# Performance work log

Hardware: AMD Instinct MI355X
Metric: run time of the kernel (lower is better)

Reference implementation:

```python
import jax, jax.numpy as jnp
import numpy as np

B, C, D, L, CTX = 8, 320, 24, 77, 768
NUM_GROUPS = 32
EPS = 1e-5


def setup_inputs() -> dict:
    key = jax.random.key(0)
    ks = jax.random.split(key, 8)
    s = 0.02
    return {
        "x": jax.random.normal(ks[0], (B, C, D, D, D), jnp.float32),
        "context": jax.random.normal(ks[1], (B, L, CTX), jnp.float32),
        "Wq": jax.random.normal(ks[2], (C, C), jnp.float32) * s,
        "bq": jnp.zeros((C,), jnp.float32),
        "Wk": jax.random.normal(ks[3], (C, CTX), jnp.float32) * s,
        "bk": jnp.zeros((C,), jnp.float32),
        "Wv": jax.random.normal(ks[4], (C, CTX), jnp.float32) * s,
        "bv": jnp.zeros((C,), jnp.float32),
        "Wo": jax.random.normal(ks[5], (C, C), jnp.float32) * s,
        "bo": jnp.zeros((C,), jnp.float32),
        "gamma": jnp.ones((C,), jnp.float32),
        "beta": jnp.zeros((C,), jnp.float32),
    }


def reference(x, context, Wq, bq, Wk, bk, Wv, bv, Wo, bo, gamma, beta):
    b, c = x.shape[:2]
    spatial = x.shape[2:]
    xf = x.reshape(b, c, -1)                                # [B, C, N]
    # 1x1 Conv3d == per-position channel matmul
    q = jnp.einsum('oc,bcn->bon', Wq, xf) + bq[None, :, None]
    ctx_t = context.transpose(0, 2, 1)                      # [B, CTX, L]
    k = jnp.einsum('oc,bcl->bol', Wk, ctx_t) + bk[None, :, None]
    v = jnp.einsum('oc,bcl->bol', Wv, ctx_t) + bv[None, :, None]
    # scores [B, N, L], scaled by C^-0.5 (int(C) in the original)
    qk = jnp.einsum('bcn,bcl->bnl', q, k) * (float(c) ** -0.5)
    w = jax.nn.softmax(qk, axis=-1)
    h = jnp.einsum('bcl,bnl->bcn', v, w)                    # [B, C, N]
    h = jnp.einsum('oc,bcn->bon', Wo, h) + bo[None, :, None]
    xr = h + xf                                             # residual
    # GroupNorm over (C/G, spatial) per group
    g = NUM_GROUPS
    xg = xr.reshape(b, g, -1)
    mu = jnp.mean(xg, axis=-1, keepdims=True)
    var = jnp.var(xg, axis=-1, keepdims=True)
    xn = ((xg - mu) * jax.lax.rsqrt(var + EPS)).reshape(b, c, -1)
    xn = xn * gamma[None, :, None] + beta[None, :, None]
    out = xn * jax.nn.sigmoid(xn)                           # Swish
    return out.reshape(b, c, *spatial)
```

## Files before the change

### kernel.cpp

```cpp
#include <hip/hip_runtime.h>
#include <hip/hip_bf16.h>

#define B_ 8
#define C_ 320
#define N_ 13824
#define NT 128
#define L_ 77
#define LP 80
#define LV 96
#define CTXD 768
#define CPG 10
#define EPS_ 1e-5f
#define SCALE_ 0.05590169943749474f
#define WTP 120

typedef __attribute__((__ext_vector_type__(4))) float f32x4;
typedef __attribute__((__ext_vector_type__(8))) short s16x8;

#define WS_ACCUM 0
#define WS_T     2048
#define WS_KST   4608
#define WS_VST   414208
#define WS_K2T   823808
#define WS_V2    1233408
#define WS_WQT   1724928
#define WS_WO    1929728

__device__ __forceinline__ unsigned short f2bf(float f) {
  union { float f; unsigned u; } v; v.f = f;
  unsigned r = v.u + 0x7FFFu + ((v.u >> 16) & 1u);
  return (unsigned short)(r >> 16);
}
__device__ __forceinline__ float bf2f(unsigned short s) {
  union { unsigned u; float f; } v; v.u = ((unsigned)s) << 16;
  return v.f;
}
__device__ __forceinline__ s16x8 cvt8(const float* p) {
  f32x4 a = *reinterpret_cast<const f32x4*>(p);
  f32x4 b = *reinterpret_cast<const f32x4*>(p + 4);
  s16x8 r;
  r[0] = (short)f2bf(a[0]); r[1] = (short)f2bf(a[1]);
  r[2] = (short)f2bf(a[2]); r[3] = (short)f2bf(a[3]);
  r[4] = (short)f2bf(b[0]); r[5] = (short)f2bf(b[1]);
  r[6] = (short)f2bf(b[2]); r[7] = (short)f2bf(b[3]);
  return r;
}
__device__ __forceinline__ f32x4 MFMA(s16x8 a, s16x8 b, f32x4 c) {
  return __builtin_amdgcn_mfma_f32_16x16x32_bf16(a, b, c, 0, 0, 0);
}

__global__ __launch_bounds__(256) void prep_kernel(const float* __restrict__ Wq,
                                                   const float* __restrict__ Wo,
                                                   const float* __restrict__ ctx,
                                                   const float* __restrict__ Wk,
                                                   const float* __restrict__ bk,
                                                   const float* __restrict__ Wv,
                                                   const float* __restrict__ bv,
                                                   unsigned short* __restrict__ wqT,
                                                   unsigned short* __restrict__ wo_bf,
                                                   unsigned short* __restrict__ kst,
                                                   unsigned short* __restrict__ vst,
                                                   float* __restrict__ zws) {
  int bid = blockIdx.x;
  if (bid < 400) {
    int t = bid * 256 + threadIdx.x;
    if (t >= C_ * C_) return;
    int o = t / C_, c = t - o * C_;
    wqT[c * C_ + o] = f2bf(Wq[t]);
    wo_bf[t] = f2bf(Wo[t]);
    return;
  }
  int kb = bid - 400;
  { int t = kb * 256 + threadIdx.x; if (t < 1152) zws[t] = 0.f; }
  int lt = kb % 5;
  int kb5 = kb / 5;
  int b = kb5 / 5;
  int oc = kb5 % 5;
  int w = threadIdx.x >> 6, lane = threadIdx.x & 63;
  int r = lane & 15, h = lane >> 4;
  int o_row = oc * 64 + w * 16 + r;
  int l = lt * 16 + r;
  bool lok = (l < L_);
  f32x4 ak = {}, av = {};
  for (int ks = 0; ks < 24; ++ks) {
    int c0 = ks * 32 + h * 8;
    s16x8 aWk = cvt8(Wk + o_row * CTXD + c0);
    s16x8 aWv = cvt8(Wv + o_row * CTXD + c0);
    s16x8 bfr = {0,0,0,0,0,0,0,0};
    if (lok) bfr = cvt8(ctx + (b * L_ + l) * CTXD + c0);
    ak = MFMA(aWk, bfr, ak);
    av = MFMA(aWv, bfr, av);
  }
#pragma unroll
  for (int j = 0; j < 4; ++j) {
    int o = oc * 64 + w * 16 + h * 4 + j;
    float bkv = bk[o], bvv = bv[o];
    unsigned short kw = lok ? f2bf(SCALE_ * (ak[j] + bkv)) : (unsigned short)0;
    unsigned short vw = lok ? f2bf(av[j] + bvv) : (unsigned short)0;
    kst[(b * LP + l) * C_ + o] = kw;
    vst[(b * LP + l) * C_ + o] = vw;
  }
}

__global__ __launch_bounds__(256) void kv2_kernel(const unsigned short* __restrict__ wqT,
                                                  const unsigned short* __restrict__ wo_bf,
                                                  const unsigned short* __restrict__ kst,
                                                  const unsigned short* __restrict__ vst,
                                                  const float* __restrict__ bq,
                                                  float* __restrict__ tbuf,
                                                  unsigned short* __restrict__ k2T,
                                                  unsigned short* __restrict__ v2) {
  int b = blockIdx.x / 5;
  int cc = blockIdx.x % 5;
  int w = threadIdx.x >> 6, lane = threadIdx.x & 63;
  int r = lane & 15, h = lane >> 4;
  int c_row = cc * 64 + w * 16 + r;
  f32x4 a2[5] = {}, av[5] = {};
#pragma unroll
  for (int ks = 0; ks < 10; ++ks) {
    int o0 = ks * 32 + h * 8;
    s16x8 aq = *reinterpret_cast<const s16x8*>(wqT + c_row * C_ + o0);
    s16x8 ao = *reinterpret_cast<const s16x8*>(wo_bf + c_row * C_ + o0);
#pragma unroll
    for (int nt = 0; nt < 5; ++nt) {
      int l = nt * 16 + r;
      s16x8 bk_ = *reinterpret_cast<const s16x8*>(kst + (b * LP + l) * C_ + o0);
      s16x8 bv_ = *reinterpret_cast<const s16x8*>(vst + (b * LP + l) * C_ + o0);
      a2[nt] = MFMA(aq, bk_, a2[nt]);
      av[nt] = MFMA(ao, bv_, av[nt]);
    }
  }
#pragma unroll
  for (int j = 0; j < 4; ++j) {
    int c = cc * 64 + w * 16 + h * 4 + j;
#pragma unroll
    for (int nt = 0; nt < 5; ++nt) {
      int l = nt * 16 + r;
      k2T[(b * LP + l) * C_ + c] = f2bf(a2[nt][j]);
      v2[(b * C_ + c) * LV + l] = f2bf(av[nt][j]);
    }
  }
  {
    int c = cc * 64 + w * 16 + (lane >> 2);
    int l = 80 + (lane & 3) * 4;
    unsigned long long* p = (unsigned long long*)(v2 + ((long)(b * C_ + c)) * LV + l);
    *p = 0ull;
  }
  if (cc == 0 && threadIdx.x < LP) {
    int l = threadIdx.x;
    float acc = 0.f;
    for (int o8 = 0; o8 < C_; o8 += 8) {
      s16x8 kv = *reinterpret_cast<const s16x8*>(kst + (b * LP + l) * C_ + o8);
#pragma unroll
      for (int j = 0; j < 8; ++j) acc += bq[o8 + j] * bf2f((unsigned short)kv[j]);
    }
    tbuf[b * LP + l] = acc;
  }
}

__global__ __launch_bounds__(512, 3) void main_kernel(const float* __restrict__ x,
                                                      const unsigned short* __restrict__ k2T,
                                                      const unsigned short* __restrict__ v2,
                                                      const float* __restrict__ tbuf,
                                                      const float* __restrict__ bo,
                                                      float* __restrict__ accum,
                                                      float* __restrict__ hout) {
  __shared__ __align__(16) unsigned short wT[NT][WTP];
  __shared__ float ch[2][C_][2];
  int bid = blockIdx.x;
  int swz = (bid & 7) * 108 + (bid >> 3);
  int b = swz / 108;
  int n0 = (swz % 108) * NT;
  int tid = threadIdx.x;
  int w = tid >> 6, lane = tid & 63, r = lane & 15, h = lane >> 4;
  const float* xg = x + (long)b * C_ * N_ + n0;
  const unsigned short* k2b = k2T + (long)b * LP * C_;
  const float* xrow = xg + w * 16 + r;

  f32x4 sacc[5] = {};
  float xvA[8], xvB[8];
#pragma unroll
  for (int j = 0; j < 8; ++j) xvA[j] = xrow[(long)(h * 8 + j) * N_];
#pragma unroll
  for (int j = 0; j < 8; ++j) xvB[j] = xrow[(long)(32 + h * 8 + j) * N_];

#define SCHUNK(KS, XV)                                                          \
  {                                                                             \
    s16x8 a;                                                                    \
    _Pragma("unroll") for (int j = 0; j < 8; ++j) a[j] = (short)f2bf(XV[j]);    \
    if (KS < 8) {                                                               \
      _Pragma("unroll") for (int j = 0; j < 8; ++j)                             \
          XV[j] = xrow[(long)((KS + 2) * 32 + h * 8 + j) * N_];                 \
    }                                                                           \
    _Pragma("unroll") for (int nt = 0; nt < 5; ++nt) {                          \
      s16x8 kf = *reinterpret_cast<const s16x8*>(                               \
          k2b + (nt * 16 + r) * C_ + KS * 32 + h * 8);                          \
      sacc[nt] = MFMA(a, kf, sacc[nt]);                                         \
    }                                                                           \
  }
  SCHUNK(0, xvA) SCHUNK(1, xvB) SCHUNK(2, xvA) SCHUNK(3, xvB) SCHUNK(4, xvA)
  SCHUNK(5, xvB) SCHUNK(6, xvA) SCHUNK(7, xvB) SCHUNK(8, xvA) SCHUNK(9, xvB)
#undef SCHUNK

#pragma unroll
  for (int nt = 0; nt < 5; ++nt) {
    float tl = tbuf[b * LP + nt * 16 + r];
#pragma unroll
    for (int j = 0; j < 4; ++j) sacc[nt][j] += tl;
  }
  bool maskpad = (r >= 13);
#pragma unroll
  for (int j = 0; j < 4; ++j) {
    float m = -1e30f;
#pragma unroll
    for (int nt = 0; nt < 5; ++nt) {
      float v = (nt == 4 && maskpad) ? -1e30f : sacc[nt][j];
      m = fmaxf(m, v);
    }
    for (int d = 1; d < 16; d <<= 1) m = fmaxf(m, __shfl_xor(m, d));
    float e[5]; float sum = 0.f;
#pragma unroll
    for (int nt = 0; nt < 5; ++nt) {
      float v = (nt == 4 && maskpad) ? 0.f : __expf(sacc[nt][j] - m);
      e[nt] = v; sum += v;
    }
    for (int d = 1; d < 16; d <<= 1) sum += __shfl_xor(sum, d);
    float inv = 1.f / sum;
    int n = w * 16 + h * 4 + j;
#pragma unroll
    for (int nt = 0; nt < 5; ++nt) wT[n][nt * 16 + r] = f2bf(e[nt] * inv);
  }
  {
    int row = tid >> 2, c0 = 80 + (tid & 3) * 4;
    *reinterpret_cast<unsigned*>(&wT[row][c0]) = 0u;
    *reinterpret_cast<unsigned*>(&wT[row][c0 + 2]) = 0u;
  }
  __syncthreads();

  int nh = w >> 2;
  int cc4 = w & 3;
  f32x4 acc[5][4] = {};
#pragma unroll
  for (int ks = 0; ks < 3; ++ks) {
    int l0 = ks * 32 + h * 8;
    s16x8 bfr[4];
#pragma unroll
    for (int nt = 0; nt < 4; ++nt)
      bfr[nt] = *reinterpret_cast<const s16x8*>(&wT[nh * 64 + nt * 16 + r][l0]);
#pragma unroll
    for (int mt = 0; mt < 5; ++mt) {
      int c = cc4 * 80 + mt * 16 + r;
      s16x8 a = *reinterpret_cast<const s16x8*>(v2 + ((long)(b * C_ + c)) * LV + l0);
#pragma unroll
      for (int nt = 0; nt < 4; ++nt) acc[mt][nt] = MFMA(a, bfr[nt], acc[mt][nt]);
    }
  }
#pragma unroll
  for (int mt = 0; mt < 5; ++mt) {
    int cb = cc4 * 80 + mt * 16 + h * 4;
    float bov[4];
#pragma unroll
    for (int j = 0; j < 4; ++j) bov[j] = bo[cb + j];
    float sv[4] = {0.f, 0.f, 0.f, 0.f}, sq[4] = {0.f, 0.f, 0.f, 0.f};
#pragma unroll
    for (int nt = 0; nt < 4; ++nt) {
      int n = nh * 64 + nt * 16 + r;
      const float* xp = xg + (long)cb * N_ + n;
#pragma unroll
      for (int j = 0; j < 4; ++j) {
        float val = acc[mt][nt][j] + bov[j] + xp[(long)j * N_];
        long e = ((long)b * C_ + cb + j) * N_ + n0 + n;
        *reinterpret_cast<unsigned short*>(
            (char*)hout + ((e >> 11) << 13) + ((e & 2047) << 1)) = f2bf(val);
        sv[j] += val; sq[j] += val * val;
      }
    }
#pragma unroll
    for (int j = 0; j < 4; ++j) {
      for (int d = 1; d < 16; d <<= 1) {
        sv[j] += __shfl_xor(sv[j], d);
        sq[j] += __shfl_xor(sq[j], d);
      }
      if (r == 0) { ch[nh][cb + j][0] = sv[j]; ch[nh][cb + j][1] = sq[j]; }
    }
  }
  __syncthreads();
  if (tid < 32) {
    float s0 = 0.f, s1 = 0.f;
#pragma unroll
    for (int i = 0; i < CPG; ++i) {
      int c = tid * CPG + i;
      s0 += ch[0][c][0] + ch[1][c][0];
      s1 += ch[0][c][1] + ch[1][c][1];
    }
    atomicAdd(&accum[b * 64 + tid * 2], s0);
    atomicAdd(&accum[b * 64 + tid * 2 + 1], s1);
  }
}

__global__ __launch_bounds__(256) void norm_kernel(float* __restrict__ hout,
                                                   const float* __restrict__ accum,
                                                   const float* __restrict__ gamma,
                                                   const float* __restrict__ beta) {
  long idx0 = (long)blockIdx.x * 2048;
  int t = threadIdx.x;
  s16x8 hv = *reinterpret_cast<const s16x8*>((const char*)hout + idx0 * 4 + t * 16);
  __syncthreads();
  long idx = idx0 + (long)t * 8;
  int b = (int)(idx / ((long)C_ * N_));
  long rem = idx - (long)b * C_ * N_;
  int c = (int)(rem / N_);
  int g = c / CPG;
  float s0 = accum[b * 64 + g * 2], s1 = accum[b * 64 + g * 2 + 1];
  const float invc = 1.f / 138240.f;
  float mu = s0 * invc;
  float var = s1 * invc - mu * mu;
  float rstd = rsqrtf(var + EPS_);
  float ga = gamma[c], be = beta[c];
  f32x4 v0, v1;
#pragma unroll
  for (int q = 0; q < 4; ++q) {
    float y = (bf2f((unsigned short)hv[q]) - mu) * rstd * ga + be;
    v0[q] = y / (1.f + __expf(-y));
    float z = (bf2f((unsigned short)hv[q + 4]) - mu) * rstd * ga + be;
    v1[q] = z / (1.f + __expf(-z));
  }
  *reinterpret_cast<f32x4*>(hout + idx) = v0;
  *reinterpret_cast<f32x4*>(hout + idx + 4) = v1;
}

extern "C" void kernel_launch(void* const* d_in, const int* in_sizes, int n_in,
                              void* d_out, int out_size, void* d_ws, size_t ws_size,
                              hipStream_t stream) {
  const float* x     = (const float*)d_in[0];
  const float* ctx   = (const float*)d_in[1];
  const float* Wq    = (const float*)d_in[2];
  const float* bq    = (const float*)d_in[3];
  const float* Wk    = (const float*)d_in[4];
  const float* bk    = (const float*)d_in[5];
  const float* Wv    = (const float*)d_in[6];
  const float* bv    = (const float*)d_in[7];
  const float* Wo    = (const float*)d_in[8];
  const float* bo    = (const float*)d_in[9];
  const float* gamma = (const float*)d_in[10];
  const float* beta  = (const float*)d_in[11];
  float* out = (float*)d_out;
  char* ws = (char*)d_ws;

  float* accum = (float*)(ws + WS_ACCUM);
  float* tbuf  = (float*)(ws + WS_T);
  unsigned short* kst  = (unsigned short*)(ws + WS_KST);
  unsigned short* vst  = (unsigned short*)(ws + WS_VST);
  unsigned short* k2T  = (unsigned short*)(ws + WS_K2T);
  unsigned short* v2   = (unsigned short*)(ws + WS_V2);
  unsigned short* wqT  = (unsigned short*)(ws + WS_WQT);
  unsigned short* wo_b = (unsigned short*)(ws + WS_WO);

  prep_kernel<<<dim3(600), dim3(256), 0, stream>>>(Wq, Wo, ctx, Wk, bk, Wv, bv,
                                                   wqT, wo_b, kst, vst, (float*)ws);
  kv2_kernel<<<dim3(40), dim3(256), 0, stream>>>(wqT, wo_b, kst, vst, bq, tbuf, k2T, v2);
  main_kernel<<<dim3(864), dim3(512), 0, stream>>>(x, k2T, v2, tbuf, bo, accum, out);
  norm_kernel<<<dim3(17280), dim3(256), 0, stream>>>(out, accum, gamma, beta);
}
```

Baseline: 194.4 us.

## Software-pipeline x, K and V loads and prefetch residual tiles in fused attention kernel

Deepens the software pipeline in the score GEMM by triple-buffering x rows and double-buffering K fragments in registers, so global loads are issued one or two chunks ahead of the MFMAs that use them. In the PV GEMM, the next V fragment is loaded before the current MFMAs run. The residual x values are prefetched into registers, with the first tile loaded before the barrier and later tiles double-buffered across the epilogue loop. The aim is to hide global memory latency behind compute, at the cost of many more live registers, which may reduce occupancy or cause spills.

```diff
diff --git a/kernel.cpp b/kernel.cpp
--- a/kernel.cpp
+++ b/kernel.cpp
@@ -178,28 +178,38 @@
   const float* xrow = xg + w * 16 + r;
 
   f32x4 sacc[5] = {};
-  float xvA[8], xvB[8];
-#pragma unroll
-  for (int j = 0; j < 8; ++j) xvA[j] = xrow[(long)(h * 8 + j) * N_];
-#pragma unroll
-  for (int j = 0; j < 8; ++j) xvB[j] = xrow[(long)(32 + h * 8 + j) * N_];
-
-#define SCHUNK(KS, XV)                                                          \
-  {                                                                             \
-    s16x8 a;                                                                    \
-    _Pragma("unroll") for (int j = 0; j < 8; ++j) a[j] = (short)f2bf(XV[j]);    \
-    if (KS < 8) {                                                               \
-      _Pragma("unroll") for (int j = 0; j < 8; ++j)                             \
-          XV[j] = xrow[(long)((KS + 2) * 32 + h * 8 + j) * N_];                 \
-    }                                                                           \
-    _Pragma("unroll") for (int nt = 0; nt < 5; ++nt) {                          \
-      s16x8 kf = *reinterpret_cast<const s16x8*>(                               \
-          k2b + (nt * 16 + r) * C_ + KS * 32 + h * 8);                          \
-      sacc[nt] = MFMA(a, kf, sacc[nt]);                                         \
-    }                                                                           \
-  }
-  SCHUNK(0, xvA) SCHUNK(1, xvB) SCHUNK(2, xvA) SCHUNK(3, xvB) SCHUNK(4, xvA)
-  SCHUNK(5, xvB) SCHUNK(6, xvA) SCHUNK(7, xvB) SCHUNK(8, xvA) SCHUNK(9, xvB)
+  float xv0[8], xv1[8], xv2[8];
+#pragma unroll
+  for (int j = 0; j < 8; ++j) xv0[j] = xrow[(long)(h * 8 + j) * N_];
+#pragma unroll
+  for (int j = 0; j < 8; ++j) xv1[j] = xrow[(long)(32 + h * 8 + j) * N_];
+#pragma unroll
+  for (int j = 0; j < 8; ++j) xv2[j] = xrow[(long)(64 + h * 8 + j) * N_];
+  s16x8 kfA[5], kfB[5];
+#pragma unroll
+  for (int nt = 0; nt < 5; ++nt)
+    kfA[nt] = *reinterpret_cast<const s16x8*>(k2b + (nt * 16 + r) * C_ + h * 8);
+
+#define SCHUNK(KS, XV, KC, KN)                                                   \
+  {                                                                              \
+    s16x8 a;                                                                     \
+    _Pragma("unroll") for (int j = 0; j < 8; ++j) a[j] = (short)f2bf(XV[j]);     \
+    if (KS < 7) {                                                                \
+      _Pragma("unroll") for (int j = 0; j < 8; ++j)                              \
+          XV[j] = xrow[(long)((KS + 3) * 32 + h * 8 + j) * N_];                  \
+    }                                                                            \
+    if (KS < 9) {                                                                \
+      _Pragma("unroll") for (int nt = 0; nt < 5; ++nt)                           \
+          KN[nt] = *reinterpret_cast<const s16x8*>(                              \
+              k2b + (nt * 16 + r) * C_ + (KS + 1) * 32 + h * 8);                 \
+    }                                                                            \
+    _Pragma("unroll") for (int nt = 0; nt < 5; ++nt)                             \
+      sacc[nt] = MFMA(a, KC[nt], sacc[nt]);                                      \
+  }
+  SCHUNK(0, xv0, kfA, kfB) SCHUNK(1, xv1, kfB, kfA) SCHUNK(2, xv2, kfA, kfB)
+  SCHUNK(3, xv0, kfB, kfA) SCHUNK(4, xv1, kfA, kfB) SCHUNK(5, xv2, kfB, kfA)
+  SCHUNK(6, xv0, kfA, kfB) SCHUNK(7, xv1, kfB, kfA) SCHUNK(8, xv2, kfA, kfB)
+  SCHUNK(9, xv0, kfB, kfA)
 #undef SCHUNK
 
 #pragma unroll
@@ -235,11 +245,21 @@
     *reinterpret_cast<unsigned*>(&wT[row][c0]) = 0u;
     *reinterpret_cast<unsigned*>(&wT[row][c0 + 2]) = 0u;
   }
-  __syncthreads();
 
   int nh = w >> 2;
   int cc4 = w & 3;
+  float rs0[16], rs1[16];
+#pragma unroll
+  for (int nt = 0; nt < 4; ++nt)
+#pragma unroll
+    for (int j = 0; j < 4; ++j)
+      rs0[nt * 4 + j] =
+          xg[(long)(cc4 * 80 + h * 4 + j) * N_ + nh * 64 + nt * 16 + r];
+  __syncthreads();
+
+  const unsigned short* v2b = v2 + (long)b * C_ * LV;
   f32x4 acc[5][4] = {};
+  s16x8 va = *reinterpret_cast<const s16x8*>(v2b + (long)(cc4 * 80 + r) * LV + h * 8);
 #pragma unroll
   for (int ks = 0; ks < 3; ++ks) {
     int l0 = ks * 32 + h * 8;
@@ -249,14 +269,30 @@
       bfr[nt] = *reinterpret_cast<const s16x8*>(&wT[nh * 64 + nt * 16 + r][l0]);
 #pragma unroll
     for (int mt = 0; mt < 5; ++mt) {
-      int c = cc4 * 80 + mt * 16 + r;
-      s16x8 a = *reinterpret_cast<const s16x8*>(v2 + ((long)(b * C_ + c)) * LV + l0);
-#pragma unroll
-      for (int nt = 0; nt < 4; ++nt) acc[mt][nt] = MFMA(a, bfr[nt], acc[mt][nt]);
+      s16x8 vn;
+      if (!(ks == 2 && mt == 4)) {
+        int ks2 = (mt == 4) ? ks + 1 : ks;
+        int mt2 = (mt == 4) ? 0 : mt + 1;
+        vn = *reinterpret_cast<const s16x8*>(
+            v2b + (long)(cc4 * 80 + mt2 * 16 + r) * LV + ks2 * 32 + h * 8);
+      }
+#pragma unroll
+      for (int nt = 0; nt < 4; ++nt) acc[mt][nt] = MFMA(va, bfr[nt], acc[mt][nt]);
+      if (!(ks == 2 && mt == 4)) va = vn;
     }
   }
 #pragma unroll
   for (int mt = 0; mt < 5; ++mt) {
+    float* rc = (mt & 1) ? rs1 : rs0;
+    float* rn = (mt & 1) ? rs0 : rs1;
+    if (mt < 4) {
+#pragma unroll
+      for (int nt = 0; nt < 4; ++nt)
+#pragma unroll
+        for (int j = 0; j < 4; ++j)
+          rn[nt * 4 + j] = xg[(long)(cc4 * 80 + (mt + 1) * 16 + h * 4 + j) * N_ +
+                              nh * 64 + nt * 16 + r];
+    }
     int cb = cc4 * 80 + mt * 16 + h * 4;
     float bov[4];
 #pragma unroll
@@ -265,10 +301,9 @@
 #pragma unroll
     for (int nt = 0; nt < 4; ++nt) {
       int n = nh * 64 + nt * 16 + r;
-      const float* xp = xg + (long)cb * N_ + n;
 #pragma unroll
       for (int j = 0; j < 4; ++j) {
-        float val = acc[mt][nt][j] + bov[j] + xp[(long)j * N_];
+        float val = acc[mt][nt][j] + bov[j] + rc[nt * 4 + j];
         long e = ((long)b * C_ + cb + j) * N_ + n0 + n;
         *reinterpret_cast<unsigned short*>(
             (char*)hout + ((e >> 11) << 13) + ((e & 2047) << 1)) = f2bf(val);
```

Result: slower. 206.9 us (+6.4%).

## Shrink main kernel to single-wave blocks of sixteen positions each

Applied to the files above, without the earlier changes.

The attention main kernel is restructured from 512-thread blocks covering 128 positions into 64-thread single-wave blocks covering 16 positions, launched as 6912 blocks. This removes the block-level __syncthreads and the two-stage shared-memory reduction, and each wave computes all 320 output channels for its positions. In exchange, the k2T and v2 operands are reloaded from global memory by eight times as many blocks. Group-statistic atomics also rise eightfold, and the explicit software prefetch of x is dropped.

```diff
diff --git a/kernel.cpp b/kernel.cpp
--- a/kernel.cpp
+++ b/kernel.cpp
@@ -4,7 +4,7 @@
 #define B_ 8
 #define C_ 320
 #define N_ 13824
-#define NT 128
+#define NB 16
 #define L_ 77
 #define LP 80
 #define LV 96
@@ -158,49 +158,36 @@
   }
 }
 
-__global__ __launch_bounds__(512, 3) void main_kernel(const float* __restrict__ x,
-                                                      const unsigned short* __restrict__ k2T,
-                                                      const unsigned short* __restrict__ v2,
-                                                      const float* __restrict__ tbuf,
-                                                      const float* __restrict__ bo,
-                                                      float* __restrict__ accum,
-                                                      float* __restrict__ hout) {
-  __shared__ __align__(16) unsigned short wT[NT][WTP];
-  __shared__ float ch[2][C_][2];
+__global__ __launch_bounds__(64, 3) void main_kernel(const float* __restrict__ x,
+                                                     const unsigned short* __restrict__ k2T,
+                                                     const unsigned short* __restrict__ v2,
+                                                     const float* __restrict__ tbuf,
+                                                     const float* __restrict__ bo,
+                                                     float* __restrict__ accum,
+                                                     float* __restrict__ hout) {
+  __shared__ __align__(16) unsigned short wT[NB][WTP];
+  __shared__ float ch[C_][2];
   int bid = blockIdx.x;
-  int swz = (bid & 7) * 108 + (bid >> 3);
-  int b = swz / 108;
-  int n0 = (swz % 108) * NT;
-  int tid = threadIdx.x;
-  int w = tid >> 6, lane = tid & 63, r = lane & 15, h = lane >> 4;
+  int b = bid & 7;
+  int n0 = (bid >> 3) * NB;
+  int lane = threadIdx.x & 63, r = lane & 15, h = lane >> 4;
   const float* xg = x + (long)b * C_ * N_ + n0;
   const unsigned short* k2b = k2T + (long)b * LP * C_;
-  const float* xrow = xg + w * 16 + r;
+  const unsigned short* v2b = v2 + (long)b * C_ * LV;
+  const float* xrow = xg + r;
 
   f32x4 sacc[5] = {};
-  float xvA[8], xvB[8];
-#pragma unroll
-  for (int j = 0; j < 8; ++j) xvA[j] = xrow[(long)(h * 8 + j) * N_];
-#pragma unroll
-  for (int j = 0; j < 8; ++j) xvB[j] = xrow[(long)(32 + h * 8 + j) * N_];
-
-#define SCHUNK(KS, XV)                                                          \
-  {                                                                             \
-    s16x8 a;                                                                    \
-    _Pragma("unroll") for (int j = 0; j < 8; ++j) a[j] = (short)f2bf(XV[j]);    \
-    if (KS < 8) {                                                               \
-      _Pragma("unroll") for (int j = 0; j < 8; ++j)                             \
-          XV[j] = xrow[(long)((KS + 2) * 32 + h * 8 + j) * N_];                 \
-    }                                                                           \
-    _Pragma("unroll") for (int nt = 0; nt < 5; ++nt) {                          \
-      s16x8 kf = *reinterpret_cast<const s16x8*>(                               \
-          k2b + (nt * 16 + r) * C_ + KS * 32 + h * 8);                          \
-      sacc[nt] = MFMA(a, kf, sacc[nt]);                                         \
-    }                                                                           \
-  }
-  SCHUNK(0, xvA) SCHUNK(1, xvB) SCHUNK(2, xvA) SCHUNK(3, xvB) SCHUNK(4, xvA)
-  SCHUNK(5, xvB) SCHUNK(6, xvA) SCHUNK(7, xvB) SCHUNK(8, xvA) SCHUNK(9, xvB)
-#undef SCHUNK
+#pragma unroll
+  for (int ks = 0; ks < 10; ++ks) {
+    s16x8 a;
+#pragma unroll
+    for (int j = 0; j < 8; ++j) a[j] = (short)f2bf(xrow[(long)(ks * 32 + h * 8 + j) * N_]);
+#pragma unroll
+    for (int nt = 0; nt < 5; ++nt) {
+      s16x8 kf = *reinterpret_cast<const s16x8*>(k2b + (nt * 16 + r) * C_ + ks * 32 + h * 8);
+      sacc[nt] = MFMA(a, kf, sacc[nt]);
+    }
+  }
 
 #pragma unroll
   for (int nt = 0; nt < 5; ++nt) {
@@ -226,75 +213,56 @@
     }
     for (int d = 1; d < 16; d <<= 1) sum += __shfl_xor(sum, d);
     float inv = 1.f / sum;
-    int n = w * 16 + h * 4 + j;
+    int n = h * 4 + j;
 #pragma unroll
     for (int nt = 0; nt < 5; ++nt) wT[n][nt * 16 + r] = f2bf(e[nt] * inv);
   }
   {
-    int row = tid >> 2, c0 = 80 + (tid & 3) * 4;
-    *reinterpret_cast<unsigned*>(&wT[row][c0]) = 0u;
-    *reinterpret_cast<unsigned*>(&wT[row][c0 + 2]) = 0u;
-  }
-  __syncthreads();
-
-  int nh = w >> 2;
-  int cc4 = w & 3;
-  f32x4 acc[5][4] = {};
-#pragma unroll
-  for (int ks = 0; ks < 3; ++ks) {
-    int l0 = ks * 32 + h * 8;
-    s16x8 bfr[4];
-#pragma unroll
-    for (int nt = 0; nt < 4; ++nt)
-      bfr[nt] = *reinterpret_cast<const s16x8*>(&wT[nh * 64 + nt * 16 + r][l0]);
-#pragma unroll
-    for (int mt = 0; mt < 5; ++mt) {
-      int c = cc4 * 80 + mt * 16 + r;
-      s16x8 a = *reinterpret_cast<const s16x8*>(v2 + ((long)(b * C_ + c)) * LV + l0);
-#pragma unroll
-      for (int nt = 0; nt < 4; ++nt) acc[mt][nt] = MFMA(a, bfr[nt], acc[mt][nt]);
-    }
-  }
-#pragma unroll
-  for (int mt = 0; mt < 5; ++mt) {
-    int cb = cc4 * 80 + mt * 16 + h * 4;
-    float bov[4];
-#pragma unroll
-    for (int j = 0; j < 4; ++j) bov[j] = bo[cb + j];
-    float sv[4] = {0.f, 0.f, 0.f, 0.f}, sq[4] = {0.f, 0.f, 0.f, 0.f};
-#pragma unroll
-    for (int nt = 0; nt < 4; ++nt) {
-      int n = nh * 64 + nt * 16 + r;
-      const float* xp = xg + (long)cb * N_ + n;
+    int row = lane >> 2, c0 = 80 + (lane & 3) * 4;
+    *reinterpret_cast<unsigned long long*>(&wT[row][c0]) = 0ull;
+  }
+
+#pragma unroll
+  for (int half = 0; half < 2; ++half) {
+    f32x4 acc[10] = {};
+#pragma unroll
+    for (int ks = 0; ks < 3; ++ks) {
+      s16x8 bfr = *reinterpret_cast<const s16x8*>(&wT[r][ks * 32 + h * 8]);
+#pragma unroll
+      for (int ct = 0; ct < 10; ++ct) {
+        int c = half * 160 + ct * 16 + r;
+        s16x8 va = *reinterpret_cast<const s16x8*>(v2b + (long)c * LV + ks * 32 + h * 8);
+        acc[ct] = MFMA(va, bfr, acc[ct]);
+      }
+    }
+#pragma unroll
+    for (int ct = 0; ct < 10; ++ct) {
+      int cb = half * 160 + ct * 16 + h * 4;
+      float sv[4], sq[4];
 #pragma unroll
       for (int j = 0; j < 4; ++j) {
-        float val = acc[mt][nt][j] + bov[j] + xp[(long)j * N_];
-        long e = ((long)b * C_ + cb + j) * N_ + n0 + n;
+        float val = acc[ct][j] + bo[cb + j] + xg[(long)(cb + j) * N_ + r];
+        long e = ((long)b * C_ + cb + j) * N_ + n0 + r;
         *reinterpret_cast<unsigned short*>(
             (char*)hout + ((e >> 11) << 13) + ((e & 2047) << 1)) = f2bf(val);
-        sv[j] += val; sq[j] += val * val;
+        sv[j] = val; sq[j] = val * val;
       }
-    }
-#pragma unroll
-    for (int j = 0; j < 4; ++j) {
-      for (int d = 1; d < 16; d <<= 1) {
-        sv[j] += __shfl_xor(sv[j], d);
-        sq[j] += __shfl_xor(sq[j], d);
+#pragma unroll
+      for (int j = 0; j < 4; ++j) {
+        for (int d = 1; d < 16; d <<= 1) {
+          sv[j] += __shfl_xor(sv[j], d);
+          sq[j] += __shfl_xor(sq[j], d);
+        }
+        if (r == 0) { ch[cb + j][0] = sv[j]; ch[cb + j][1] = sq[j]; }
       }
-      if (r == 0) { ch[nh][cb + j][0] = sv[j]; ch[nh][cb + j][1] = sq[j]; }
-    }
-  }
-  __syncthreads();
-  if (tid < 32) {
+    }
+  }
+  if (lane < 32) {
     float s0 = 0.f, s1 = 0.f;
 #pragma unroll
-    for (int i = 0; i < CPG; ++i) {
-      int c = tid * CPG + i;
-      s0 += ch[0][c][0] + ch[1][c][0];
-      s1 += ch[0][c][1] + ch[1][c][1];
-    }
-    atomicAdd(&accum[b * 64 + tid * 2], s0);
-    atomicAdd(&accum[b * 64 + tid * 2 + 1], s1);
+    for (int i = 0; i < CPG; ++i) { s0 += ch[lane * CPG + i][0]; s1 += ch[lane * CPG + i][1]; }
+    atomicAdd(&accum[b * 64 + lane * 2], s0);
+    atomicAdd(&accum[b * 64 + lane * 2 + 1], s1);
   }
 }
 
@@ -359,6 +327,6 @@
   prep_kernel<<<dim3(600), dim3(256), 0, stream>>>(Wq, Wo, ctx, Wk, bk, Wv, bv,
                                                    wqT, wo_b, kst, vst, (float*)ws);
   kv2_kernel<<<dim3(40), dim3(256), 0, stream>>>(wqT, wo_b, kst, vst, bq, tbuf, k2T, v2);
-  main_kernel<<<dim3(864), dim3(512), 0, stream>>>(x, k2T, v2, tbuf, bo, accum, out);
+  main_kernel<<<dim3(6912), dim3(64), 0, stream>>>(x, k2T, v2, tbuf, bo, accum, out);
   norm_kernel<<<dim3(17280), dim3(256), 0, stream>>>(out, accum, gamma, beta);
 }
```

Result: slower. 214.5 us (+10.3%).

## Pre-transpose x to bf16 position-major layout and fragment-order K for main kernel

Applied to the files above, without the earlier changes.

Adds a separate kernel that converts x to bf16 and transposes it to [B, N, C], so the main kernel reads contiguous 16-byte MFMA A-fragments instead of strided fp32 column loads. K2 is written in MFMA fragment order and double-buffered in registers, and V fragment loads are software-prefetched one step ahead. The residual now uses the bf16 copy of x, which lowers its precision. The extra pass reads all of x once and writes a bf16 copy, adding traffic and a launch, and the occupancy hint changes to waves_per_eu(2,3).

```diff
diff --git a/kernel.cpp b/kernel.cpp
--- a/kernel.cpp
+++ b/kernel.cpp
@@ -16,15 +16,17 @@
 
 typedef __attribute__((__ext_vector_type__(4))) float f32x4;
 typedef __attribute__((__ext_vector_type__(8))) short s16x8;
+typedef __attribute__((__ext_vector_type__(4))) unsigned short u16x4;
 
 #define WS_ACCUM 0
 #define WS_T     2048
 #define WS_KST   4608
 #define WS_VST   414208
-#define WS_K2T   823808
+#define WS_K2F   823808
 #define WS_V2    1233408
 #define WS_WQT   1724928
 #define WS_WO    1929728
+#define WS_XT    2134528
 
 __device__ __forceinline__ unsigned short f2bf(float f) {
   union { float f; unsigned u; } v; v.f = f;
@@ -47,6 +49,31 @@
 }
 __device__ __forceinline__ f32x4 MFMA(s16x8 a, s16x8 b, f32x4 c) {
   return __builtin_amdgcn_mfma_f32_16x16x32_bf16(a, b, c, 0, 0, 0);
+}
+
+__global__ __launch_bounds__(256) void xpose_kernel(const float* __restrict__ x,
+                                                    unsigned short* __restrict__ xT) {
+  __shared__ __align__(16) unsigned short tile[64][336];
+  int bid = blockIdx.x;
+  int b = bid & 7;
+  int t0 = (bid >> 3) * 64;
+  int tid = threadIdx.x;
+  int nq = (tid & 15) * 4;
+  int cc = tid >> 4;
+  const float* xb = x + (long)b * C_ * N_ + t0;
+#pragma unroll
+  for (int it = 0; it < 20; ++it) {
+    int c = it * 16 + cc;
+    f32x4 v = *reinterpret_cast<const f32x4*>(xb + (long)c * N_ + nq);
+#pragma unroll
+    for (int q = 0; q < 4; ++q) tile[nq + q][c] = f2bf(v[q]);
+  }
+  __syncthreads();
+  int row = tid >> 2, part = tid & 3;
+  const s16x8* src = reinterpret_cast<const s16x8*>(&tile[row][part * 80]);
+  s16x8* dst = reinterpret_cast<s16x8*>(xT + ((long)b * N_ + t0 + row) * C_ + part * 80);
+#pragma unroll
+  for (int k = 0; k < 10; ++k) dst[k] = src[k];
 }
 
 __global__ __launch_bounds__(256) void prep_kernel(const float* __restrict__ Wq,
@@ -108,7 +135,7 @@
                                                   const unsigned short* __restrict__ vst,
                                                   const float* __restrict__ bq,
                                                   float* __restrict__ tbuf,
-                                                  unsigned short* __restrict__ k2T,
+                                                  unsigned short* __restrict__ k2F,
                                                   unsigned short* __restrict__ v2) {
   int b = blockIdx.x / 5;
   int cc = blockIdx.x % 5;
@@ -133,10 +160,11 @@
 #pragma unroll
   for (int j = 0; j < 4; ++j) {
     int c = cc * 64 + w * 16 + h * 4 + j;
+    int ks2 = c >> 5, h2 = (c >> 3) & 3, j2 = c & 7;
 #pragma unroll
     for (int nt = 0; nt < 5; ++nt) {
       int l = nt * 16 + r;
-      k2T[(b * LP + l) * C_ + c] = f2bf(a2[nt][j]);
+      k2F[(((b * 5 + nt) * 10 + ks2) << 9) + ((h2 * 16 + r) << 3) + j2] = f2bf(a2[nt][j]);
       v2[(b * C_ + c) * LV + l] = f2bf(av[nt][j]);
     }
   }
@@ -158,13 +186,15 @@
   }
 }
 
-__global__ __launch_bounds__(512, 3) void main_kernel(const float* __restrict__ x,
-                                                      const unsigned short* __restrict__ k2T,
-                                                      const unsigned short* __restrict__ v2,
-                                                      const float* __restrict__ tbuf,
-                                                      const float* __restrict__ bo,
-                                                      float* __restrict__ accum,
-                                                      float* __restrict__ hout) {
+__global__ __launch_bounds__(512)
+__attribute__((amdgpu_waves_per_eu(2, 3)))
+void main_kernel(const unsigned short* __restrict__ xT,
+                 const unsigned short* __restrict__ k2F,
+                 const unsigned short* __restrict__ v2,
+                 const float* __restrict__ tbuf,
+                 const float* __restrict__ bo,
+                 float* __restrict__ accum,
+                 float* __restrict__ hout) {
   __shared__ __align__(16) unsigned short wT[NT][WTP];
   __shared__ float ch[2][C_][2];
   int bid = blockIdx.x;
@@ -173,33 +203,31 @@
   int n0 = (swz % 108) * NT;
   int tid = threadIdx.x;
   int w = tid >> 6, lane = tid & 63, r = lane & 15, h = lane >> 4;
-  const float* xg = x + (long)b * C_ * N_ + n0;
-  const unsigned short* k2b = k2T + (long)b * LP * C_;
-  const float* xrow = xg + w * 16 + r;
+  const unsigned short* xTb = xT + ((long)b * N_ + n0) * C_;
+  const unsigned short* xTn = xTb + (long)(w * 16 + r) * C_;
+  const unsigned short* k2f = k2F + ((long)b * 50 << 9);
 
   f32x4 sacc[5] = {};
-  float xvA[8], xvB[8];
-#pragma unroll
-  for (int j = 0; j < 8; ++j) xvA[j] = xrow[(long)(h * 8 + j) * N_];
-#pragma unroll
-  for (int j = 0; j < 8; ++j) xvB[j] = xrow[(long)(32 + h * 8 + j) * N_];
-
-#define SCHUNK(KS, XV)                                                          \
+  s16x8 kfA[5], kfB[5];
+#pragma unroll
+  for (int nt = 0; nt < 5; ++nt)
+    kfA[nt] = *reinterpret_cast<const s16x8*>(k2f + ((nt * 10) << 9) + (lane << 3));
+
+#define SCHUNK(KS, KC, KN)                                                      \
   {                                                                             \
-    s16x8 a;                                                                    \
-    _Pragma("unroll") for (int j = 0; j < 8; ++j) a[j] = (short)f2bf(XV[j]);    \
-    if (KS < 8) {                                                               \
-      _Pragma("unroll") for (int j = 0; j < 8; ++j)                             \
-          XV[j] = xrow[(long)((KS + 2) * 32 + h * 8 + j) * N_];                 \
+    s16x8 a = *reinterpret_cast<const s16x8*>(xTn + KS * 32 + h * 8);           \
+    if (KS < 9) {                                                               \
+      _Pragma("unroll") for (int nt = 0; nt < 5; ++nt)                          \
+          KN[nt] = *reinterpret_cast<const s16x8*>(                             \
+              k2f + ((nt * 10 + KS + 1) << 9) + (lane << 3));                   \
     }                                                                           \
-    _Pragma("unroll") for (int nt = 0; nt < 5; ++nt) {                          \
-      s16x8 kf = *reinterpret_cast<const s16x8*>(                               \
-          k2b + (nt * 16 + r) * C_ + KS * 32 + h * 8);                          \
-      sacc[nt] = MFMA(a, kf, sacc[nt]);                                         \
-    }                                                                           \
-  }
-  SCHUNK(0, xvA) SCHUNK(1, xvB) SCHUNK(2, xvA) SCHUNK(3, xvB) SCHUNK(4, xvA)
-  SCHUNK(5, xvB) SCHUNK(6, xvA) SCHUNK(7, xvB) SCHUNK(8, xvA) SCHUNK(9, xvB)
+    _Pragma("unroll") for (int nt = 0; nt < 5; ++nt)                            \
+      sacc[nt] = MFMA(a, KC[nt], sacc[nt]);                                     \
+  }
+  SCHUNK(0, kfA, kfB) SCHUNK(1, kfB, kfA) SCHUNK(2, kfA, kfB)
+  SCHUNK(3, kfB, kfA) SCHUNK(4, kfA, kfB) SCHUNK(5, kfB, kfA)
+  SCHUNK(6, kfA, kfB) SCHUNK(7, kfB, kfA) SCHUNK(8, kfA, kfB)
+  SCHUNK(9, kfB, kfA)
 #undef SCHUNK
 
 #pragma unroll
@@ -239,7 +267,9 @@
 
   int nh = w >> 2;
   int cc4 = w & 3;
+  const unsigned short* v2b = v2 + (long)b * C_ * LV;
   f32x4 acc[5][4] = {};
+  s16x8 va = *reinterpret_cast<const s16x8*>(v2b + (long)(cc4 * 80 + r) * LV + h * 8);
 #pragma unroll
   for (int ks = 0; ks < 3; ++ks) {
     int l0 = ks * 32 + h * 8;
@@ -249,10 +279,16 @@
       bfr[nt] = *reinterpret_cast<const s16x8*>(&wT[nh * 64 + nt * 16 + r][l0]);
 #pragma unroll
     for (int mt = 0; mt < 5; ++mt) {
-      int c = cc4 * 80 + mt * 16 + r;
-      s16x8 a = *reinterpret_cast<const s16x8*>(v2 + ((long)(b * C_ + c)) * LV + l0);
-#pragma unroll
-      for (int nt = 0; nt < 4; ++nt) acc[mt][nt] = MFMA(a, bfr[nt], acc[mt][nt]);
+      s16x8 vn;
+      if (!(ks == 2 && mt == 4)) {
+        int ks2 = (mt == 4) ? ks + 1 : ks;
+        int mt2 = (mt == 4) ? 0 : mt + 1;
+        vn = *reinterpret_cast<const s16x8*>(
+            v2b + (long)(cc4 * 80 + mt2 * 16 + r) * LV + ks2 * 32 + h * 8);
+      }
+#pragma unroll
+      for (int nt = 0; nt < 4; ++nt) acc[mt][nt] = MFMA(va, bfr[nt], acc[mt][nt]);
+      if (!(ks == 2 && mt == 4)) va = vn;
     }
   }
 #pragma unroll
@@ -265,10 +301,10 @@
 #pragma unroll
     for (int nt = 0; nt < 4; ++nt) {
       int n = nh * 64 + nt * 16 + r;
-      const float* xp = xg + (long)cb * N_ + n;
+      u16x4 xr = *reinterpret_cast<const u16x4*>(xTb + (long)n * C_ + cb);
 #pragma unroll
       for (int j = 0; j < 4; ++j) {
-        float val = acc[mt][nt][j] + bov[j] + xp[(long)j * N_];
+        float val = acc[mt][nt][j] + bov[j] + bf2f(xr[j]);
         long e = ((long)b * C_ + cb + j) * N_ + n0 + n;
         *reinterpret_cast<unsigned short*>(
             (char*)hout + ((e >> 11) << 13) + ((e & 2047) << 1)) = f2bf(val);
@@ -351,14 +387,16 @@
   float* tbuf  = (float*)(ws + WS_T);
   unsigned short* kst  = (unsigned short*)(ws + WS_KST);
   unsigned short* vst  = (unsigned short*)(ws + WS_VST);
-  unsigned short* k2T  = (unsigned short*)(ws + WS_K2T);
+  unsigned short* k2F  = (unsigned short*)(ws + WS_K2F);
   unsigned short* v2   = (unsigned short*)(ws + WS_V2);
   unsigned short* wqT  = (unsigned short*)(ws + WS_WQT);
   unsigned short* wo_b = (unsigned short*)(ws + WS_WO);
-
+  unsigned short* xT   = (unsigned short*)(ws + WS_XT);
+
+  xpose_kernel<<<dim3(1728), dim3(256), 0, stream>>>(x, xT);
   prep_kernel<<<dim3(600), dim3(256), 0, stream>>>(Wq, Wo, ctx, Wk, bk, Wv, bv,
                                                    wqT, wo_b, kst, vst, (float*)ws);
-  kv2_kernel<<<dim3(40), dim3(256), 0, stream>>>(wqT, wo_b, kst, vst, bq, tbuf, k2T, v2);
-  main_kernel<<<dim3(864), dim3(512), 0, stream>>>(x, k2T, v2, tbuf, bo, accum, out);
+  kv2_kernel<<<dim3(40), dim3(256), 0, stream>>>(wqT, wo_b, kst, vst, bq, tbuf, k2F, v2);
+  main_kernel<<<dim3(864), dim3(512), 0, stream>>>(xT, k2F, v2, tbuf, bo, accum, out);
   norm_kernel<<<dim3(17280), dim3(256), 0, stream>>>(out, accum, gamma, beta);
 }
```

New measurement: 213.8 us. +10.0%, slower.
